# Optimization experiments

Hardware: AMD Instinct MI355X
Metric: run time of the kernel (lower is better)

Reference implementation:

```python
import jax, jax.numpy as jnp
import numpy as np

N = 20000      # cells (nodes)
E = 640000     # kNN edges (before self loops)
IN = 2000      # gene features
C = 64         # out_channels
H = 4          # attention heads
NEG_SLOPE = 0.2
EPS = 1e-12


def setup_inputs() -> dict:
    key = jax.random.key(0)
    ks = jax.random.split(key, 12)
    s = lambda k, shape, sc: (jax.random.normal(k, shape, jnp.float32) * sc)
    x = s(ks[0], (N, IN), 1.0)
    edge_index = jax.random.randint(ks[1], (2, E), 0, N)
    W_ae = s(ks[2], (IN, C), 0.02); b_ae = jnp.zeros((C,), jnp.float32)
    Wl = s(ks[3], (C, H * C), 0.1); bl = jnp.zeros((H * C,), jnp.float32)
    Wr = s(ks[4], (C, H * C), 0.1); br = jnp.zeros((H * C,), jnp.float32)
    att = s(ks[5], (H, C), 0.1)
    b_conv = jnp.zeros((H * C,), jnp.float32)
    W_lin = s(ks[6], (H * C, C), 0.1); b_lin = jnp.zeros((C,), jnp.float32)
    ln_w = jnp.ones((C,), jnp.float32); ln_b = jnp.zeros((C,), jnp.float32)
    return dict(x=x, edge_index=edge_index, W_ae=W_ae, b_ae=b_ae, Wl=Wl, bl=bl,
                Wr=Wr, br=br, att=att, b_conv=b_conv, W_lin=W_lin, b_lin=b_lin,
                ln_w=ln_w, ln_b=ln_b)


def reference(x, edge_index, W_ae, b_ae, Wl, bl, Wr, br, att, b_conv,
              W_lin, b_lin, ln_w, ln_b):
    # Encoder.AE: linear projection of gene features -> node embeddings
    h = x @ W_ae + b_ae                              # [N, C]

    # GATv2Conv (PyG defaults: add_self_loops=True, negative_slope=0.2,
    # dropout is identity at eval, concat=True)
    loops = jnp.arange(N)
    src = jnp.concatenate([edge_index[0], loops])    # [E+N] message sources j
    dst = jnp.concatenate([edge_index[1], loops])    # [E+N] targets i

    xl = (h @ Wl + bl).reshape(N, H, C)              # W_l x (source features)
    xr = (h @ Wr + br).reshape(N, H, C)              # W_r x (target features)

    g = jax.nn.leaky_relu(xl[src] + xr[dst], NEG_SLOPE)   # [E+N, H, C]
    logits = jnp.einsum('ehc,hc->eh', g, att)             # [E+N, H]

    # segment softmax over incoming edges of each target node
    m = jax.ops.segment_max(logits, dst, num_segments=N)  # [N, H]
    e = jnp.exp(logits - m[dst])
    denom = jax.ops.segment_sum(e, dst, num_segments=N)   # [N, H] (>0: self loops)
    alpha = e / denom[dst]                                 # [E+N, H]

    out = jax.ops.segment_sum(alpha[:, :, None] * xl[src], dst, num_segments=N)
    out = out.reshape(N, H * C) + b_conv             # concat heads + bias

    # Encoder.linear + activation (relu), dropout = identity at eval
    a = jax.nn.relu(out @ W_lin + b_lin)             # [N, C]

    # residual + TF-style LayerNorm
    y = a + h
    u = y.mean(-1, keepdims=True)
    v = ((y - u) ** 2).mean(-1, keepdims=True)
    return ln_w * (y - u) / jnp.sqrt(v + EPS) + ln_b
```

## Files before the change

kernel.cpp:

```cpp
#include <hip/hip_runtime.h>
#include <hip/hip_fp16.h>

#define N_NODES 20000
#define N_EDGES 640000
#define IN_F    2000
#define KPAD    2048
#define C_OUT   64
#define HC      256
#define NEG     0.2f
#define SCAN_B  79

typedef __attribute__((ext_vector_type(4))) float f32x4;
typedef __attribute__((ext_vector_type(8))) short bf16x8;
typedef _Float16 h2 __attribute__((ext_vector_type(2)));
typedef _Float16 f16x8 __attribute__((ext_vector_type(8)));

__device__ inline unsigned short f2bf(float f) {
    unsigned u = __float_as_uint(f);
    return (unsigned short)((u + 0x7FFFu + ((u >> 16) & 1u)) >> 16);
}

__device__ inline unsigned cvt_pk_bf16(float lo, float hi) {
    unsigned r;
    asm("v_cvt_pk_bf16_f32 %0, %1, %2" : "=v"(r) : "v"(lo), "v"(hi));
    return r;
}


__global__ __launch_bounds__(256) void k_prep(
    const float* __restrict__ W_ae, unsigned short* __restrict__ Wpk,
    const float* __restrict__ W_lin, unsigned short* __restrict__ Wt16,
    const int* __restrict__ dst, int* __restrict__ counts) {
    int b = blockIdx.x, t = threadIdx.x;
    if (b < 512) {
        int idx = b * 256 + t;
        int n = idx >> 11;
        int k = idx & 2047;
        float v = (k < IN_F) ? W_ae[(size_t)k * C_OUT + n] : 0.f;
        Wpk[(size_t)(k >> 3) * 512 + n * 8 + (k & 7)] = f2bf(v);
    } else if (b < 576) {
        int idx = (b - 512) * 256 + t;
        int col = idx >> 8;
        int k = idx & 255;
        _Float16 v = (_Float16)W_lin[(size_t)k * C_OUT + col];
        Wt16[(size_t)col * HC + k] = __builtin_bit_cast(unsigned short, v);
    } else {
        int e = (b - 576) * 256 + t;
        if (e < N_EDGES) atomicAdd(&counts[dst[e]], 1);
    }
}


__global__ void k_scan1(const int* __restrict__ counts, int* __restrict__ bsum) {
    int t = threadIdx.x, b = blockIdx.x;
    int i = b * 256 + t;
    int v = (i < N_NODES) ? counts[i] : 0;
    int s = v;
    #pragma unroll
    for (int d = 1; d < 64; d <<= 1) s += __shfl_xor(s, d, 64);
    __shared__ int ws[4];
    if ((t & 63) == 0) ws[t >> 6] = s;
    __syncthreads();
    if (t == 0) bsum[b] = ws[0] + ws[1] + ws[2] + ws[3];
}

__global__ void k_scan2(const int* __restrict__ bsum, int* __restrict__ bbase,
                        int* __restrict__ offsets) {
    int lane = threadIdx.x;
    int v0 = (lane < SCAN_B) ? bsum[lane] : 0;
    int v1 = (64 + lane < SCAN_B) ? bsum[64 + lane] : 0;
    int s0 = v0;
    #pragma unroll
    for (int d = 1; d < 64; d <<= 1) { int t = __shfl_up(s0, d, 64); if (lane >= d) s0 += t; }
    int tot0 = __shfl(s0, 63, 64);
    int s1 = v1;
    #pragma unroll
    for (int d = 1; d < 64; d <<= 1) { int t = __shfl_up(s1, d, 64); if (lane >= d) s1 += t; }
    int tot1 = __shfl(s1, 63, 64);
    if (lane < SCAN_B) bbase[lane] = s0 - v0;
    if (64 + lane < SCAN_B) bbase[64 + lane] = tot0 + s1 - v1;
    if (lane == 0) offsets[N_NODES] = tot0 + tot1;
}

__global__ void k_scan3(const int* __restrict__ counts, const int* __restrict__ bbase,
                        int* __restrict__ offsets, int* __restrict__ cursor) {
    int t = threadIdx.x, b = blockIdx.x;
    int lane = t & 63, wid = t >> 6;
    int i = b * 256 + t;
    int v = (i < N_NODES) ? counts[i] : 0;
    int s = v;
    #pragma unroll
    for (int d = 1; d < 64; d <<= 1) { int u = __shfl_up(s, d, 64); if (lane >= d) s += u; }
    __shared__ int ws[4];
    if (lane == 63) ws[wid] = s;
    __syncthreads();
    int wb = 0;
    #pragma unroll
    for (int w = 0; w < 3; ++w) if (w < wid) wb += ws[w];
    int excl = bbase[b] + wb + (s - v);
    if (i < N_NODES) { offsets[i] = excl; cursor[i] = excl; }
}


__global__ __launch_bounds__(512) void k_gemm_sc(
    const float* __restrict__ x, const unsigned short* __restrict__ Wpk,
    const float* __restrict__ b, float* __restrict__ h,
    const int* __restrict__ src, const int* __restrict__ dst,
    int* __restrict__ cursor, int* __restrict__ ssrc) {
    if (blockIdx.x >= 1250) {
        int e = (blockIdx.x - 1250) * 512 + threadIdx.x;
        if (e < N_EDGES) {
            int d = dst[e];
            int p = atomicAdd(&cursor[d], 1);
            ssrc[p] = src[e];
        }
        return;
    }
    __shared__ float red[16][7][64];
    int t = threadIdx.x;
    int lane = t & 63, w = t >> 6;
    int row0 = blockIdx.x * 16;
    int r = lane & 15, kc = lane >> 4;
    const float* xrow = x + (size_t)(row0 + r) * IN_F;
    f32x4 acc[4] = {{0,0,0,0},{0,0,0,0},{0,0,0,0},{0,0,0,0}};

    int kstart = w * 256;
    #pragma unroll
    for (int s = 0; s < 8; ++s) {
        int kb = kstart + s * 32 + kc * 8;
        int kbc = kb <= 1992 ? kb : 1992;
        float4 f0 = *(const float4*)&xrow[kbc];
        float4 f1 = *(const float4*)&xrow[kbc + 4];
        uint4 uu;
        uu.x = cvt_pk_bf16(f0.x, f0.y);
        uu.y = cvt_pk_bf16(f0.z, f0.w);
        uu.z = cvt_pk_bf16(f1.x, f1.y);
        uu.w = cvt_pk_bf16(f1.z, f1.w);
        if (kb > 1992) { uu.x = 0u; uu.y = 0u; uu.z = 0u; uu.w = 0u; }
        bf16x8 af = __builtin_bit_cast(bf16x8, uu);
        const unsigned short* bp = Wpk + (size_t)(kb >> 3) * 512;
        #pragma unroll
        for (int cb = 0; cb < 4; ++cb) {
            bf16x8 bf = *(const bf16x8*)&bp[(cb * 16 + r) * 8];
            acc[cb] = __builtin_amdgcn_mfma_f32_16x16x32_bf16(af, bf, acc[cb], 0, 0, 0);
        }
    }

    if (w > 0) {
        #pragma unroll
        for (int cb = 0; cb < 4; ++cb)
            #pragma unroll
            for (int rr = 0; rr < 4; ++rr)
                red[cb * 4 + rr][w - 1][lane] = acc[cb][rr];
    }
    __syncthreads();
    if (w == 0) {
        #pragma unroll
        for (int cb = 0; cb < 4; ++cb)
            #pragma unroll
            for (int rr = 0; rr < 4; ++rr) {
                float s = acc[cb][rr];
                #pragma unroll
                for (int ww = 0; ww < 7; ++ww)
                    s += red[cb * 4 + rr][ww][lane];
                acc[cb][rr] = s;
            }
        int ci = kc * 4, cj = r;
        #pragma unroll
        for (int cb = 0; cb < 4; ++cb) {
            int col = cb * 16 + cj;
            float bb = b[col];
            #pragma unroll
            for (int rr = 0; rr < 4; ++rr)
                h[(size_t)(row0 + ci + rr) * C_OUT + col] = acc[cb][rr] + bb;
        }
    }
}


__global__ __launch_bounds__(256) void k_xlxr2(
    const float* __restrict__ h, const float* __restrict__ Wl, const float* __restrict__ bl,
    const float* __restrict__ Wr, const float* __restrict__ br,
    unsigned short* __restrict__ xlh, float* __restrict__ xr) {
    __shared__ float hs[64][68];
    __shared__ float Ws[64][128];
    int t = threadIdx.x;
    int mb = blockIdx.x >> 2, nb = blockIdx.x & 3;
    int node0 = mb * 64;
    const float* Wsrc = (nb < 2) ? (Wl + nb * 128) : (Wr + (nb - 2) * 128);
    const float* bsrc = (nb < 2) ? (bl + nb * 128) : (br + (nb - 2) * 128);

    {
        int row = t >> 2, q = t & 3;
        int gnode = node0 + row; if (gnode >= N_NODES) gnode = N_NODES - 1;
        const float4* src = (const float4*)&h[(size_t)gnode * C_OUT + q * 16];
        *(float4*)&hs[row][q * 16 + 0]  = src[0];
        *(float4*)&hs[row][q * 16 + 4]  = src[1];
        *(float4*)&hs[row][q * 16 + 8]  = src[2];
        *(float4*)&hs[row][q * 16 + 12] = src[3];
    }
    {
        #pragma unroll
        for (int i = 0; i < 8; ++i) {
            int f = t + i * 256;
            int k = f >> 5, c4 = (f & 31) << 2;
            *(float4*)&Ws[k][c4] = *(const float4*)&Wsrc[(size_t)k * HC + c4];
        }
    }
    __syncthreads();

    int tr = t >> 5;
    int tc = t & 31;
    float4 acc[8];
    float4 bv = *(const float4*)&bsrc[tc * 4];
    #pragma unroll
    for (int r = 0; r < 8; ++r) acc[r] = bv;

    for (int k4 = 0; k4 < 64; k4 += 4) {
        float4 w0 = *(float4*)&Ws[k4 + 0][tc * 4];
        float4 w1 = *(float4*)&Ws[k4 + 1][tc * 4];
        float4 w2 = *(float4*)&Ws[k4 + 2][tc * 4];
        float4 w3 = *(float4*)&Ws[k4 + 3][tc * 4];
        #pragma unroll
        for (int r = 0; r < 8; ++r) {
            float4 a = *(float4*)&hs[tr * 8 + r][k4];
            acc[r].x += a.x * w0.x + a.y * w1.x + a.z * w2.x + a.w * w3.x;
            acc[r].y += a.x * w0.y + a.y * w1.y + a.z * w2.y + a.w * w3.y;
            acc[r].z += a.x * w0.z + a.y * w1.z + a.z * w2.z + a.w * w3.z;
            acc[r].w += a.x * w0.w + a.y * w1.w + a.z * w2.w + a.w * w3.w;
        }
    }
    #pragma unroll
    for (int r = 0; r < 8; ++r) {
        int gnode = node0 + tr * 8 + r;
        if (gnode < N_NODES) {
            if (nb < 2) {
                h2 lo = { (_Float16)acc[r].x, (_Float16)acc[r].y };
                h2 hi = { (_Float16)acc[r].z, (_Float16)acc[r].w };
                uint2 o = { __builtin_bit_cast(unsigned, lo),
                            __builtin_bit_cast(unsigned, hi) };
                *(uint2*)&xlh[(size_t)gnode * HC + nb * 128 + tc * 4] = o;
            } else {
                *(float4*)&xr[(size_t)gnode * HC + (nb - 2) * 128 + tc * 4] = acc[r];
            }
        }
    }
}


__global__ __launch_bounds__(256) void k_attn(
    const unsigned short* __restrict__ xlh, const float* __restrict__ xr,
    const int* __restrict__ offsets, const int* __restrict__ ssrc,
    const float* __restrict__ att, const float* __restrict__ b_conv,
    unsigned short* __restrict__ ovh) {
    int wid = threadIdx.x >> 6, lane = threadIdx.x & 63;
    int node = blockIdx.x * 4 + wid;
    int sub = lane >> 4;
    int sl  = lane & 15;
    int c0  = sl * 16;

    const h2 z2  = { (_Float16)0.f, (_Float16)0.f };
    const h2 ns2 = { (_Float16)NEG, (_Float16)NEG };

    h2 xr2[8], at2[8];
    #pragma unroll
    for (int i = 0; i < 4; ++i) {
        float4 t4 = *(const float4*)&xr[(size_t)node * HC + c0 + i * 4];
        xr2[i*2+0] = h2{ (_Float16)t4.x, (_Float16)t4.y };
        xr2[i*2+1] = h2{ (_Float16)t4.z, (_Float16)t4.w };
        float4 a4 = *(const float4*)&att[c0 + i * 4];
        at2[i*2+0] = h2{ (_Float16)a4.x, (_Float16)a4.y };
        at2[i*2+1] = h2{ (_Float16)a4.z, (_Float16)a4.w };
    }
    h2 acc2[8];
    #pragma unroll
    for (int i = 0; i < 8; ++i) acc2[i] = z2;
    float denom = 0.f;

    auto load_edge = [&](int j, uint4& w0, uint4& w1) {
        const uint4* rp = (const uint4*)&xlh[(size_t)j * HC + c0];
        w0 = rp[0]; w1 = rp[1];
    };
    auto compute_edge = [&](uint4 w0, uint4 w1, bool valid) {
        h2 x2[8];
        x2[0] = __builtin_bit_cast(h2, w0.x); x2[1] = __builtin_bit_cast(h2, w0.y);
        x2[2] = __builtin_bit_cast(h2, w0.z); x2[3] = __builtin_bit_cast(h2, w0.w);
        x2[4] = __builtin_bit_cast(h2, w1.x); x2[5] = __builtin_bit_cast(h2, w1.y);
        x2[6] = __builtin_bit_cast(h2, w1.z); x2[7] = __builtin_bit_cast(h2, w1.w);
        h2 p2 = z2;
        #pragma unroll
        for (int i = 0; i < 8; ++i) {
            h2 g  = x2[i] + xr2[i];
            h2 gs = g * ns2;
            g = __builtin_elementwise_max(g, gs);
            p2 += g * at2[i];
        }
        float p = (float)p2.x + (float)p2.y;
        p += __shfl_xor(p, 1); p += __shfl_xor(p, 2);
        float ex = valid ? __expf(p) : 0.f;
        denom += ex;
        h2 e2 = { (_Float16)ex, (_Float16)ex };
        #pragma unroll
        for (int i = 0; i < 8; ++i) acc2[i] += e2 * x2[i];
    };

    {
        uint4 s0v, s1v;
        load_edge(node, s0v, s1v);
        compute_edge(s0v, s1v, sub == 0);
    }

    int s0 = offsets[node], s1 = offsets[node + 1];
    for (int base = s0; base < s1; base += 64) {
        int rem = s1 - base;
        int cnt = rem < 64 ? rem : 64;
        int jv = (base + lane < s1) ? ssrc[base + lane] : 0;
        int niter = (cnt + 3) >> 2;
        uint4 a0, a1, b0, b1;
        int jA = __shfl(jv, sub, 64);
        load_edge(jA, a0, a1);
        for (int it = 0; it < niter; it += 2) {
            int eB = ((it + 1) << 2) + sub;
            int jB = __shfl(jv, eB & 63, 64);
            load_edge(jB, b0, b1);
            compute_edge(a0, a1, ((it << 2) + sub) < cnt);
            int eA2 = ((it + 2) << 2) + sub;
            int jA2 = __shfl(jv, eA2 & 63, 64);
            load_edge(jA2, a0, a1);
            compute_edge(b0, b1, eB < cnt);
        }
    }

    float accf[16];
    #pragma unroll
    for (int i = 0; i < 8; ++i) {
        accf[2*i]   = (float)acc2[i].x;
        accf[2*i+1] = (float)acc2[i].y;
    }
    #pragma unroll
    for (int i = 0; i < 16; ++i) {
        accf[i] += __shfl_xor(accf[i], 16);
        accf[i] += __shfl_xor(accf[i], 32);
    }
    denom += __shfl_xor(denom, 16);
    denom += __shfl_xor(denom, 32);

    float inv = 1.f / denom;
    if (sub == 0) {
        float bcf[16];
        #pragma unroll
        for (int i = 0; i < 4; ++i) {
            float4 bc = *(const float4*)&b_conv[c0 + i * 4];
            bcf[i*4+0] = bc.x; bcf[i*4+1] = bc.y; bcf[i*4+2] = bc.z; bcf[i*4+3] = bc.w;
        }
        unsigned ww[8];
        #pragma unroll
        for (int i = 0; i < 8; ++i) {
            h2 p = { (_Float16)(accf[2*i]   * inv + bcf[2*i]),
                     (_Float16)(accf[2*i+1] * inv + bcf[2*i+1]) };
            ww[i] = __builtin_bit_cast(unsigned, p);
        }
        uint4 o0 = { ww[0], ww[1], ww[2], ww[3] };
        uint4 o1 = { ww[4], ww[5], ww[6], ww[7] };
        *(uint4*)&ovh[(size_t)node * HC + c0]     = o0;
        *(uint4*)&ovh[(size_t)node * HC + c0 + 8] = o1;
    }
}


__global__ __launch_bounds__(256) void k_post(
    const unsigned short* __restrict__ ovh, const unsigned short* __restrict__ Wt16,
    const float* __restrict__ b_lin, const float* __restrict__ hbuf,
    const float* __restrict__ ln_w, const float* __restrict__ ln_b,
    float* __restrict__ out) {
    int t = threadIdx.x;
    int lane = t & 63, w = t >> 6;
    int node0 = blockIdx.x * 64 + w * 16;
    int r = lane & 15, kc = lane >> 4;
    int noder = node0 + r;
    int nodec = noder < N_NODES ? noder : N_NODES - 1;

    f32x4 acc[4] = {{0,0,0,0},{0,0,0,0},{0,0,0,0},{0,0,0,0}};
    #pragma unroll
    for (int k0 = 0; k0 < HC; k0 += 32) {
        int kb = k0 + kc * 8;
        f16x8 af = *(const f16x8*)&ovh[(size_t)nodec * HC + kb];
        #pragma unroll
        for (int cb = 0; cb < 4; ++cb) {
            f16x8 bf = *(const f16x8*)&Wt16[(size_t)(cb * 16 + r) * HC + kb];
            acc[cb] = __builtin_amdgcn_mfma_f32_16x16x32_f16(af, bf, acc[cb], 0, 0, 0);
        }
    }

    int ci = (lane >> 4) * 4, cj = lane & 15;
    #pragma unroll
    for (int rr = 0; rr < 4; ++rr) {
        int grow = node0 + ci + rr;
        int growc = grow < N_NODES ? grow : N_NODES - 1;
        float y[4];
        float ssum = 0.f;
        #pragma unroll
        for (int cb = 0; cb < 4; ++cb) {
            int col = cb * 16 + cj;
            float a = acc[cb][rr] + b_lin[col];
            a = a > 0.f ? a : 0.f;
            float yy = a + hbuf[(size_t)growc * C_OUT + col];
            y[cb] = yy;
            ssum += yy;
        }
        ssum += __shfl_xor(ssum, 1); ssum += __shfl_xor(ssum, 2);
        ssum += __shfl_xor(ssum, 4); ssum += __shfl_xor(ssum, 8);
        float m = ssum * (1.f / 64.f);
        float vs = 0.f;
        #pragma unroll
        for (int cb = 0; cb < 4; ++cb) { float d = y[cb] - m; vs += d * d; }
        vs += __shfl_xor(vs, 1); vs += __shfl_xor(vs, 2);
        vs += __shfl_xor(vs, 4); vs += __shfl_xor(vs, 8);
        float rinv = rsqrtf(vs * (1.f / 64.f) + 1e-12f);
        if (grow < N_NODES) {
            #pragma unroll
            for (int cb = 0; cb < 4; ++cb) {
                int col = cb * 16 + cj;
                out[(size_t)grow * C_OUT + col] =
                    ln_w[col] * (y[cb] - m) * rinv + ln_b[col];
            }
        }
    }
}


extern "C" void kernel_launch(void* const* d_in, const int* in_sizes, int n_in,
                              void* d_out, int out_size, void* d_ws, size_t ws_size,
                              hipStream_t stream) {
    const float* x     = (const float*)d_in[0];
    const int*   ei    = (const int*)  d_in[1];
    const float* W_ae  = (const float*)d_in[2];
    const float* b_ae  = (const float*)d_in[3];
    const float* Wl    = (const float*)d_in[4];
    const float* bl    = (const float*)d_in[5];
    const float* Wr    = (const float*)d_in[6];
    const float* br    = (const float*)d_in[7];
    const float* att   = (const float*)d_in[8];
    const float* b_conv= (const float*)d_in[9];
    const float* W_lin = (const float*)d_in[10];
    const float* b_lin = (const float*)d_in[11];
    const float* ln_w  = (const float*)d_in[12];
    const float* ln_b  = (const float*)d_in[13];
    float* out = (float*)d_out;
    const int* src = ei;
    const int* dst = ei + N_EDGES;

    char* ws = (char*)d_ws;
    size_t off = 0;
    auto alloc = [&](size_t bytes) {
        void* p = ws + off;
        off = (off + bytes + 255) & ~(size_t)255;
        return p;
    };
    float* h       = (float*)alloc((size_t)N_NODES * C_OUT * 4);
    unsigned short* xlh = (unsigned short*)alloc((size_t)N_NODES * HC * 2);
    float* xr      = (float*)alloc((size_t)N_NODES * HC * 4);
    unsigned short* ovh = (unsigned short*)alloc((size_t)N_NODES * HC * 2);
    int*   counts  = (int*)  alloc((size_t)N_NODES * 4);
    int*   offsets = (int*)  alloc((size_t)(N_NODES + 1) * 4);
    int*   cursor  = (int*)  alloc((size_t)N_NODES * 4);
    int*   ssrc    = (int*)  alloc((size_t)N_EDGES * 4);
    unsigned short* Wpk  = (unsigned short*)alloc((size_t)C_OUT * KPAD * 2);
    unsigned short* Wt16 = (unsigned short*)alloc((size_t)C_OUT * HC * 2);
    int*   bsum    = (int*)  alloc((size_t)SCAN_B * 4);
    int*   bbase   = (int*)  alloc((size_t)SCAN_B * 4);

    (void)hipMemsetAsync(counts, 0, (size_t)N_NODES * 4, stream);
    k_prep   <<<576 + (N_EDGES + 255) / 256, 256, 0, stream>>>(W_ae, Wpk, W_lin, Wt16,
                                                               dst, counts);
    k_scan1  <<<SCAN_B, 256, 0, stream>>>(counts, bsum);
    k_scan2  <<<1, 64, 0, stream>>>(bsum, bbase, offsets);
    k_scan3  <<<SCAN_B, 256, 0, stream>>>(counts, bbase, offsets, cursor);
    k_gemm_sc<<<2500, 512, 0, stream>>>(x, Wpk, b_ae, h, src, dst, cursor, ssrc);
    k_xlxr2  <<<((N_NODES + 63) / 64) * 4, 256, 0, stream>>>(h, Wl, bl, Wr, br, xlh, xr);
    k_attn   <<<N_NODES / 4, 256, 0, stream>>>(xlh, xr, offsets, ssrc, att, b_conv, ovh);
    k_post   <<<(N_NODES + 63) / 64, 256, 0, stream>>>(ovh, Wt16, b_lin, h,
                                                       ln_w, ln_b, out);
}
```

Measured before the change: 183.1 us.

## Stage x tile in swizzled LDS and split GEMM warps by column tile

The encoder GEMM now loads each 16-row x tile cooperatively with coalesced float4 reads, converts it to bf16 and stores it in XOR-swizzled shared memory. Each of the 8 waves then computes one 16-column output tile over half of K, instead of every wave covering all 64 columns over a K-slice. This cuts the 7-way cross-wave reduction to a single 2-way LDS reduction and improves global load coalescing of x. The cost is two extra barriers per K iteration and a serialised load/compute pattern with no overlap between them.

Result: no change. 183.7 us (+0.3%).

```diff
diff --git a/kernel.cpp b/kernel.cpp
--- a/kernel.cpp
+++ b/kernel.cpp
@@ -116,63 +116,58 @@
         }
         return;
     }
-    __shared__ float red[16][7][64];
+    __shared__ unsigned short Asw[16][64][8];
+    __shared__ float red[4][16][17];
     int t = threadIdx.x;
     int lane = t & 63, w = t >> 6;
     int row0 = blockIdx.x * 16;
     int r = lane & 15, kc = lane >> 4;
-    const float* xrow = x + (size_t)(row0 + r) * IN_F;
-    f32x4 acc[4] = {{0,0,0,0},{0,0,0,0},{0,0,0,0},{0,0,0,0}};
-
-    int kstart = w * 256;
-    #pragma unroll
-    for (int s = 0; s < 8; ++s) {
-        int kb = kstart + s * 32 + kc * 8;
-        int kbc = kb <= 1992 ? kb : 1992;
-        float4 f0 = *(const float4*)&xrow[kbc];
-        float4 f1 = *(const float4*)&xrow[kbc + 4];
-        uint4 uu;
-        uu.x = cvt_pk_bf16(f0.x, f0.y);
-        uu.y = cvt_pk_bf16(f0.z, f0.w);
-        uu.z = cvt_pk_bf16(f1.x, f1.y);
-        uu.w = cvt_pk_bf16(f1.z, f1.w);
-        if (kb > 1992) { uu.x = 0u; uu.y = 0u; uu.z = 0u; uu.w = 0u; }
-        bf16x8 af = __builtin_bit_cast(bf16x8, uu);
-        const unsigned short* bp = Wpk + (size_t)(kb >> 3) * 512;
-        #pragma unroll
-        for (int cb = 0; cb < 4; ++cb) {
-            bf16x8 bf = *(const bf16x8*)&bp[(cb * 16 + r) * 8];
-            acc[cb] = __builtin_amdgcn_mfma_f32_16x16x32_bf16(af, bf, acc[cb], 0, 0, 0);
-        }
-    }
-
-    if (w > 0) {
-        #pragma unroll
-        for (int cb = 0; cb < 4; ++cb)
-            #pragma unroll
-            for (int rr = 0; rr < 4; ++rr)
-                red[cb * 4 + rr][w - 1][lane] = acc[cb][rr];
+    int ct = w & 3;
+    int kh = w >> 2;
+    int srow = t >> 5;
+    int sj   = t & 31;
+    const float* xrow = x + (size_t)(row0 + srow) * IN_F;
+    f32x4 acc = {0.f, 0.f, 0.f, 0.f};
+
+    for (int it = 0; it < 4; ++it) {
+        #pragma unroll
+        for (int p = 0; p < 4; ++p) {
+            int f  = p * 128 + sj * 4;
+            int kg = it * 512 + f;
+            float4 v = {0.f, 0.f, 0.f, 0.f};
+            if (kg < IN_F) v = *(const float4*)&xrow[kg];
+            unsigned lo = cvt_pk_bf16(v.x, v.y);
+            unsigned hi = cvt_pk_bf16(v.z, v.w);
+            int c = (f >> 3) ^ srow;
+            int o = f & 7;
+            *(unsigned*)&Asw[srow][c][o]     = lo;
+            *(unsigned*)&Asw[srow][c][o + 2] = hi;
+        }
+        __syncthreads();
+        int cb0 = kh * 32;
+        #pragma unroll
+        for (int s = 0; s < 8; ++s) {
+            int cki = cb0 + s * 4 + kc;
+            bf16x8 af = *(bf16x8*)&Asw[r][cki ^ r][0];
+            int gch = it * 64 + cki;
+            bf16x8 bf = *(const bf16x8*)&Wpk[(size_t)gch * 512 + (ct * 16 + r) * 8];
+            acc = __builtin_amdgcn_mfma_f32_16x16x32_bf16(af, bf, acc, 0, 0, 0);
+        }
+        __syncthreads();
+    }
+
+    int ci = (lane >> 4) * 4, cj = lane & 15;
+    if (kh == 1) {
+        #pragma unroll
+        for (int rr = 0; rr < 4; ++rr) red[ct][ci + rr][cj] = acc[rr];
     }
     __syncthreads();
-    if (w == 0) {
-        #pragma unroll
-        for (int cb = 0; cb < 4; ++cb)
-            #pragma unroll
-            for (int rr = 0; rr < 4; ++rr) {
-                float s = acc[cb][rr];
-                #pragma unroll
-                for (int ww = 0; ww < 7; ++ww)
-                    s += red[cb * 4 + rr][ww][lane];
-                acc[cb][rr] = s;
-            }
-        int ci = kc * 4, cj = r;
-        #pragma unroll
-        for (int cb = 0; cb < 4; ++cb) {
-            int col = cb * 16 + cj;
-            float bb = b[col];
-            #pragma unroll
-            for (int rr = 0; rr < 4; ++rr)
-                h[(size_t)(row0 + ci + rr) * C_OUT + col] = acc[cb][rr] + bb;
+    if (kh == 0) {
+        float bb = b[ct * 16 + cj];
+        #pragma unroll
+        for (int rr = 0; rr < 4; ++rr) {
+            float s = acc[rr] + red[ct][ci + rr][cj] + bb;
+            h[(size_t)(row0 + ci + rr) * C_OUT + ct * 16 + cj] = s;
         }
     }
 }
```
